# Optimization experiments

Measured on AMD Instinct MI355X. Metric: run time of the kernel, lower is better.

Reference implementation:

```python
import jax, jax.numpy as jnp
import numpy as np
from jax import lax

# program token ids
PAD, START, END, SCENE, INTERSECT, FILT, RELATE, QUERY = range(8)
SKIP = (PAD, START, END)


def conv2d(x, w, b, dil=1):
    # 'same' padding for odd kernels (3x3 pad=dil, 1x1 pad=0), NCHW/OIHW
    pad = dil * (w.shape[2] // 2)
    y = lax.conv_general_dilated(x, w, (1, 1), [(pad, pad), (pad, pad)],
                                 rhs_dilation=(dil, dil),
                                 dimension_numbers=('NCHW', 'OIHW', 'NCHW'))
    return y + b[None, :, None, None]


def maxpool2(x):
    return lax.reduce_window(x, -jnp.inf, lax.max, (1, 1, 2, 2), (1, 1, 2, 2), 'VALID')


def exec_program(prog, feat_input, p):
    """Run one (concrete) program over a batch of stem features. prog: tuple of ints,
    executed in reversed order exactly like TbDNet.forward."""
    B, _, H, W = feat_input.shape
    output = feat_input
    saved = None
    for t in reversed(prog):
        if t in SKIP:
            continue
        if t == SCENE:
            saved = output
            output = jnp.ones((B, 1, H, W), feat_input.dtype)
        elif t == INTERSECT:  # AndModule: elementwise min of attentions
            output = jnp.minimum(output, saved)
        elif t == FILT:
            a = feat_input * output  # [B,D,H,W] * [B,1,H,W]
            a = jax.nn.relu(conv2d(a, p['att_w1'], p['att_b1']))
            a = jax.nn.relu(conv2d(a, p['att_w2'], p['att_b2']))
            output = jax.nn.sigmoid(conv2d(a, p['att_w3'], p['att_b3']))
        elif t == RELATE:  # RelateModule: dilated conv stack (1,2,4,8,1) -> conv1x1 sigmoid
            a = feat_input * output
            for w, b, d in ((p['rel_w1'], p['rel_b1'], 1), (p['rel_w2'], p['rel_b2'], 2),
                            (p['rel_w3'], p['rel_b3'], 4), (p['rel_w4'], p['rel_b4'], 8),
                            (p['rel_w5'], p['rel_b5'], 1)):
                a = jax.nn.relu(conv2d(a, w, b, d))
            output = jax.nn.sigmoid(conv2d(a, p['rel_w6'], p['rel_b6']))
        elif t == QUERY:
            a = feat_input * output
            a = jax.nn.relu(conv2d(a, p['qry_w1'], p['qry_b1']))
            output = jax.nn.relu(conv2d(a, p['qry_w2'], p['qry_b2']))
    return output


def tbd_forward(feats, programs_np, p):
    B = feats.shape[0]
    stem = jax.nn.relu(conv2d(feats, p['stem_w1'], p['stem_b1']))
    stem = jax.nn.relu(conv2d(stem, p['stem_w2'], p['stem_b2']))  # [B,D,H,W]
    D, H, W = stem.shape[1], stem.shape[2], stem.shape[3]
    # group samples by identical program so dispatch runs batched, not per-sample
    groups = {}
    for n in range(B):
        groups.setdefault(tuple(int(v) for v in programs_np[n]), []).append(n)
    mod_out = jnp.zeros((B, D, H, W), feats.dtype)
    for prog, idxs in groups.items():
        idx = jnp.array(idxs)
        mod_out = mod_out.at[idx].set(exec_program(prog, stem[idx], p))
    # classifier: conv1x1 -> relu -> maxpool2 -> flatten -> fc -> relu -> fc
    x = jax.nn.relu(conv2d(mod_out, p['cls_w'], p['cls_b']))
    x = maxpool2(x)                        # [B,1024,7,7]
    x = x.reshape(B, -1)                   # [B,50176]
    x = jax.nn.relu(x @ p['fc1_w'].T + p['fc1_b'])
    return x @ p['fc2_w'].T + p['fc2_b']   # [B,28]


def setup_inputs() -> dict:
    key = jax.random.key(0)
    ks = iter(jax.random.split(key, 64))
    def rn(shape, s=0.05):
        return jax.random.normal(next(ks), shape, dtype=jnp.float32) * s
    B, Cin, H, W, D, P, L, A = 64, 1024, 14, 14, 128, 1024, 1024, 28
    feats = jax.random.normal(next(ks), (B, Cin, H, W), dtype=jnp.float32)
    # stored programs; execution order is reversed(stored)
    progA = [START, QUERY, FILT, RELATE, FILT, SCENE, END, PAD]            # scene->filter->relate->filter->query
    progB = [START, QUERY, INTERSECT, FILT, SCENE, FILT, SCENE, END]       # two filter branches -> intersect -> query
    programs = jnp.array([progA] * (B // 2) + [progB] * (B // 2), dtype=jnp.int32)
    inp = {'feats': feats, 'programs': programs,
           'stem_w1': rn((D, Cin, 3, 3), 0.02), 'stem_b1': rn((D,)),
           'stem_w2': rn((D, D, 3, 3)), 'stem_b2': rn((D,)),
           'att_w1': rn((D, D, 3, 3)), 'att_b1': rn((D,)),
           'att_w2': rn((D, D, 3, 3)), 'att_b2': rn((D,)),
           'att_w3': rn((1, D, 1, 1)), 'att_b3': rn((1,)),
           'rel_w1': rn((D, D, 3, 3)), 'rel_b1': rn((D,)),
           'rel_w2': rn((D, D, 3, 3)), 'rel_b2': rn((D,)),
           'rel_w3': rn((D, D, 3, 3)), 'rel_b3': rn((D,)),
           'rel_w4': rn((D, D, 3, 3)), 'rel_b4': rn((D,)),
           'rel_w5': rn((D, D, 3, 3)), 'rel_b5': rn((D,)),
           'rel_w6': rn((1, D, 1, 1)), 'rel_b6': rn((1,)),
           'qry_w1': rn((D, D, 3, 3)), 'qry_b1': rn((D,)),
           'qry_w2': rn((D, D, 3, 3)), 'qry_b2': rn((D,)),
           'cls_w': rn((P, D, 1, 1)), 'cls_b': rn((P,)),
           'fc1_w': rn((L, P * (H // 2) * (W // 2)), 0.01), 'fc1_b': rn((L,)),
           'fc2_w': rn((A, L)), 'fc2_b': rn((A,))}
    return inp


PARAM_NAMES = ['stem_w1', 'stem_b1', 'stem_w2', 'stem_b2',
               'att_w1', 'att_b1', 'att_w2', 'att_b2', 'att_w3', 'att_b3',
               'rel_w1', 'rel_b1', 'rel_w2', 'rel_b2', 'rel_w3', 'rel_b3',
               'rel_w4', 'rel_b4', 'rel_w5', 'rel_b5', 'rel_w6', 'rel_b6',
               'qry_w1', 'qry_b1', 'qry_w2', 'qry_b2',
               'cls_w', 'cls_b', 'fc1_w', 'fc1_b', 'fc2_w', 'fc2_b']


def reference(feats, programs, stem_w1, stem_b1, stem_w2, stem_b2,
              att_w1, att_b1, att_w2, att_b2, att_w3, att_b3,
              rel_w1, rel_b1, rel_w2, rel_b2, rel_w3, rel_b3,
              rel_w4, rel_b4, rel_w5, rel_b5, rel_w6, rel_b6,
              qry_w1, qry_b1, qry_w2, qry_b2,
              cls_w, cls_b, fc1_w, fc1_b, fc2_w, fc2_b):
    vals = [stem_w1, stem_b1, stem_w2, stem_b2,
            att_w1, att_b1, att_w2, att_b2, att_w3, att_b3,
            rel_w1, rel_b1, rel_w2, rel_b2, rel_w3, rel_b3,
            rel_w4, rel_b4, rel_w5, rel_b5, rel_w6, rel_b6,
            qry_w1, qry_b1, qry_w2, qry_b2,
            cls_w, cls_b, fc1_w, fc1_b, fc2_w, fc2_b]
    p = dict(zip(PARAM_NAMES, vals))
    return tbd_forward(feats, np.asarray(programs), p)
```

## Files before the change

kernel.cpp:

```cpp
#include <hip/hip_runtime.h>
#include <math.h>


typedef __attribute__((ext_vector_type(8)))  short   short8;
typedef __attribute__((ext_vector_type(8)))  __bf16  bf16x8;
typedef __attribute__((ext_vector_type(4)))  float   f32x4;

#define NROUNDS 11
#define NKS 98

#define B_WSTEM1 0UL
#define B_WSTEM2 2359296UL
#define B_WMOD   2654208UL
#define B_WCLS   5308416UL
#define B_STEM   5570560UL
#define B_XA     8781824UL
#define B_XB     11993088UL
#define B_FEAT   15204352UL
#define B_ATTN   18415616UL
#define B_SAVED  18465792UL
#define B_SCHED  18515968UL
#define B_ACTB   18520064UL
#define B_FC1T   24942592UL
#define B_P1X1   25204736UL
#define B_S1P    67108864UL
#define B_FC1P   100663296UL

__device__ __forceinline__ unsigned short f2bf(float f) {
    unsigned int b = __float_as_uint(f);
    b += 0x7fffu + ((b >> 16) & 1u);
    return (unsigned short)(b >> 16);
}
__device__ __forceinline__ float bf2f(unsigned short u) {
    return __uint_as_float(((unsigned int)u) << 16);
}
__device__ __forceinline__ f32x4 mfma16(bf16x8 a, bf16x8 b, f32x4 c) {
    return __builtin_amdgcn_mfma_f32_16x16x32_bf16(a, b, c, 0, 0, 0);
}

struct RepackArgs { const float* src[12]; };

__global__ __launch_bounds__(256) void k_repack(RepackArgs a, char* ws)
{
    const int y = blockIdx.y;
    const float* __restrict__ src = a.src[y];
    int gid = blockIdx.x * 256 + threadIdx.x;
    int gsz = gridDim.x * 256;
    if (y == 11) {
        unsigned short* dst = (unsigned short*)(ws + B_WCLS);
        for (int i = gid; i < 131072; i += gsz) dst[i] = f2bf(src[i]);
    } else {
        const int IC = (y == 0) ? 1024 : 128;
        const int lg = (y == 0) ? 10 : 7;
        unsigned short* dst = (unsigned short*)(ws + ((y == 0) ? B_WSTEM1
                                    : (y == 1) ? B_WSTEM2
                                    : B_WMOD + (size_t)(y - 2) * 294912));
        const int total = 9 << (lg + 7);
        for (int i = gid; i < total; i += gsz) {
            int ic = i & (IC - 1);
            int oc = (i >> lg) & 127;
            int t  = i >> (lg + 7);
            dst[i] = f2bf(src[((size_t)oc * IC + ic) * 9 + t]);
        }
    }
}

__global__ __launch_bounds__(256) void k_decode_init(const int* __restrict__ prog, char* ws)
{
    int gid = blockIdx.x * 256 + threadIdx.x;
    int gsz = gridDim.x * 256;
    float* attn  = (float*)(ws + B_ATTN);
    float* saved = (float*)(ws + B_SAVED);
    float* p1    = (float*)(ws + B_P1X1);
    for (int i = gid; i < 64 * 196; i += gsz) { attn[i] = 1.0f; saved[i] = 1.0f; }
    for (int i = gid; i < 8 * 64 * 196; i += gsz) p1[i] = 0.0f;
    unsigned int* fz = (unsigned int*)(ws + B_FEAT);
    for (int i = gid; i < 64 * 25088 / 2; i += gsz) fz[i] = 0u;
    if (gid < 64) {
        int n = gid;
        int ent[NROUNDS];
        for (int r = 0; r < NROUNDS; ++r) ent[r] = 0;
        int rc = 0, nslot = 0;
        int pscene = 0, pinter = 0, pmat = 0, pmw = 0;
#define PREBITS ((pscene<<17)|(pinter<<18)|(pmat<<19)|(pmw<<22))
#define CLRPRE  (pscene = pinter = pmat = pmw = 0)
#define EMIT(v) do { if (rc < NROUNDS) ent[rc++] = (v); } while (0)
        for (int j = 7; j >= 0; --j) {
            int t = prog[n * 8 + j];
            switch (t) {
                case 3: pscene = 1; break;
                case 4: pinter = 1; break;
                case 5: {
                    int e1 = 3 | (0<<4) | (1<<8) | (1<<12) | (2<<13) | (0<<15) | PREBITS;
                    CLRPRE; EMIT(e1);
                    EMIT(3 | (1<<4) | (1<<8) | (0<<12) | (0<<13) | (1<<15)
                           | (1<<23) | (0<<24) | (nslot<<25));
                    pmat = nslot + 1; pmw = 0; nslot++;
                    break;
                }
                case 6: {
                    int e1 = 3 | (2<<4) | (1<<8) | (1<<12) | (2<<13) | (0<<15) | PREBITS;
                    CLRPRE; EMIT(e1);
                    EMIT(3 | (3<<4) | (2<<8) | (0<<12) | (0<<13) | (1<<15));
                    EMIT(3 | (4<<4) | (4<<8) | (0<<12) | (1<<13) | (0<<15));
                    EMIT(3 | (5<<4) | (8<<8) | (0<<12) | (0<<13) | (1<<15));
                    EMIT(3 | (6<<4) | (1<<8) | (0<<12) | (1<<13) | (0<<15)
                           | (1<<23) | (1<<24) | (nslot<<25));
                    pmat = nslot + 1; pmw = 1; nslot++;
                    break;
                }
                case 7: {
                    int e1 = 3 | (7<<4) | (1<<8) | (1<<12) | (2<<13) | (0<<15) | PREBITS;
                    CLRPRE; EMIT(e1);
                    EMIT(3 | (8<<4) | (1<<8) | (0<<12) | (0<<13) | (2<<15));
                    break;
                }
                default: break;
            }
        }
#undef EMIT
#undef PREBITS
#undef CLRPRE
        int* sched = (int*)(ws + B_SCHED);
        for (int r = 0; r < NROUNDS; ++r) sched[n * NROUNDS + r] = ent[r];
    }
}

__global__ __launch_bounds__(512) void k_stem1p(const float* __restrict__ feats,
                                                const unsigned short* __restrict__ wrep,
                                                char* ws)
{
    __shared__ unsigned short s_img[197 * 136];
    const int bx = blockIdx.x;
    const int n = bx >> 3, ks = bx & 7;
    const int tid = threadIdx.x, lane = tid & 63;
    const int w = tid >> 6, wm = w & 1, wn = w >> 1;
    const int l15 = lane & 15, lq = lane >> 4;

    if (tid < 68) ((unsigned int*)s_img)[196 * 68 + tid] = 0u;

    int pglob[4], pbyt[4], pyv[4], pxv[4];
#pragma unroll
    for (int j = 0; j < 4; ++j) {
        int p  = (wn + 4 * j) * 16 + l15;
        pglob[j] = p;
        int py = p / 14;
        pyv[j] = (p < 196) ? py : 10000;
        pxv[j] = p - py * 14;
        pbyt[j] = p * 272 + lq * 16;
    }
    const int zaddr = 196 * 272 + lq * 16;
    const int nJ = (wn == 0) ? 4 : 3;

    f32x4 acc[4][4];
#pragma unroll
    for (int m = 0; m < 4; ++m)
#pragma unroll
        for (int j = 0; j < 4; ++j) acc[m][j] = (f32x4){0.f, 0.f, 0.f, 0.f};

    const int icg = tid & 31;
    const int qq0 = tid >> 5;
    const int icb = ks * 128;

    const float* sf = feats + ((size_t)n * 1024 + icb) * 196;
    for (int qq = qq0; qq < 49; qq += 16) {
        const float* p0 = sf + icg * 4 * 196 + qq * 4;
        float4 r0 = *(const float4*)(p0);
        float4 r1 = *(const float4*)(p0 + 196);
        float4 r2 = *(const float4*)(p0 + 392);
        float4 r3 = *(const float4*)(p0 + 588);
#pragma unroll
        for (int e = 0; e < 4; ++e) {
            uint2 v;
            v.x = (unsigned int)f2bf(((const float*)&r0)[e]) |
                  ((unsigned int)f2bf(((const float*)&r1)[e]) << 16);
            v.y = (unsigned int)f2bf(((const float*)&r2)[e]) |
                  ((unsigned int)f2bf(((const float*)&r3)[e]) << 16);
            *(uint2*)(s_img + (qq * 4 + e) * 136 + icg * 4) = v;
        }
    }
    __syncthreads();

#pragma unroll
    for (int t = 0; t < 9; ++t) {
        const int dy = t / 3 - 1, dx = t % 3 - 1;
        int baddr[4];
#pragma unroll
        for (int j = 0; j < 4; ++j) {
            int yy = pyv[j] + dy, xx = pxv[j] + dx;
            bool ok = ((unsigned)yy < 14u) && ((unsigned)xx < 14u);
            baddr[j] = ok ? (pbyt[j] + (dy * 14 + dx) * 272) : zaddr;
        }
#pragma unroll
        for (int kc = 0; kc < 4; ++kc) {
            const unsigned short* wt = wrep +
                ((size_t)(t * 128 + wm * 64 + l15) * 1024 + icb + kc * 32 + lq * 8);
            bf16x8 am[4];
#pragma unroll
            for (int m = 0; m < 4; ++m)
                am[m] = *(const bf16x8*)(wt + (size_t)m * 16 * 1024);
#pragma unroll
            for (int j = 0; j < 4; ++j) {
                if (j < nJ) {
                    bf16x8 b = *(const bf16x8*)((const char*)s_img + baddr[j] + kc * 64);
#pragma unroll
                    for (int m = 0; m < 4; ++m)
                        acc[m][j] = mfma16(am[m], b, acc[m][j]);
                }
            }
        }
    }

    unsigned short* part = (unsigned short*)(ws + B_S1P);
#pragma unroll
    for (int m = 0; m < 4; ++m) {
        const int oc = wm * 64 + m * 16 + lq * 4;
#pragma unroll
        for (int j = 0; j < 4; ++j) {
            if (j < nJ) {
                int p = pglob[j];
                if (p < 196) {
                    unsigned int lo = (unsigned int)f2bf(acc[m][j][0]) |
                                      ((unsigned int)f2bf(acc[m][j][1]) << 16);
                    unsigned int hi = (unsigned int)f2bf(acc[m][j][2]) |
                                      ((unsigned int)f2bf(acc[m][j][3]) << 16);
                    uint2 pk; pk.x = lo; pk.y = hi;
                    *(uint2*)(part + (((size_t)ks * 64 + n) * 196 + p) * 128 + oc) = pk;
                }
            }
        }
    }
}

__global__ __launch_bounds__(256) void k_stem1r(const char* __restrict__ ws_c,
                                                const float* __restrict__ bias,
                                                unsigned short* __restrict__ xa)
{
    int i = blockIdx.x * 256 + threadIdx.x;
    const unsigned short* part = (const unsigned short*)(ws_c + B_S1P);
    int oc8 = (i & 15) * 8;
    int np  = i >> 4;
    float s[8] = {};
#pragma unroll
    for (int ks = 0; ks < 8; ++ks) {
        short8 v = *(const short8*)(part + (((size_t)ks * 64) * 196 + np) * 128 + oc8);
#pragma unroll
        for (int e = 0; e < 8; ++e) s[e] += bf2f((unsigned short)v[e]);
    }
    short8 o;
#pragma unroll
    for (int e = 0; e < 8; ++e)
        o[e] = (short)f2bf(fmaxf(s[e] + bias[oc8 + e], 0.f));
    *(short8*)(xa + (size_t)np * 128 + oc8) = o;
}

__device__ void conv_core32(const unsigned short* __restrict__ srcB,
                            const float* __restrict__ s_gate,
                            const unsigned short* __restrict__ wrep,
                            const float* __restrict__ bias,
                            unsigned short* __restrict__ dst,
                            int dil, int oct, int pxh,
                            unsigned short* s_img,
                            int post, const float* __restrict__ pwv,
                            float* __restrict__ pdst)
{
    const int tid  = threadIdx.x, lane = tid & 63;
    const int w    = tid >> 6, wm = w & 1, wn = w >> 1;
    const int l15  = lane & 15, lq = lane >> 4;

    if (tid < 68) ((unsigned int*)s_img)[196 * 68 + tid] = 0u;

    int pglob[4], pbyt[4], pyv[4], pxv[4];
#pragma unroll
    for (int j = 0; j < 4; ++j) {
        int nt = wn + 2 * j;
        int p  = (pxh * 7 + nt) * 16 + l15;
        pglob[j] = p;
        int py = p / 14;
        pyv[j] = (p < 196) ? py : 10000;
        pxv[j] = p - py * 14;
        pbyt[j] = p * 272 + lq * 16;
    }
    const int zaddr = 196 * 272 + lq * 16;
    const int nNT = (wn == 0) ? 4 : 3;

    f32x4 acc[4];
#pragma unroll
    for (int j = 0; j < 4; ++j) acc[j] = (f32x4){0.f, 0.f, 0.f, 0.f};

    if (s_gate) {
        for (int i = tid; i < 196 * 16; i += 256) {
            int p = i >> 4, c8 = (i & 15) * 8;
            short8 v = *(const short8*)(srcB + p * 128 + c8);
            float g = s_gate[p];
            short8 ov;
#pragma unroll
            for (int e = 0; e < 8; ++e)
                ov[e] = (short)f2bf(bf2f((unsigned short)v[e]) * g);
            *(short8*)(s_img + p * 136 + c8) = ov;
        }
    } else {
        for (int i = tid; i < 196 * 16; i += 256) {
            int p = i >> 4, c8 = (i & 15) * 8;
            *(short8*)(s_img + p * 136 + c8) = *(const short8*)(srcB + p * 128 + c8);
        }
    }
    __syncthreads();

    const unsigned short* wlane = wrep + (size_t)(oct * 32 + wm * 16 + l15) * 128 + lq * 8;
#pragma unroll
    for (int t = 0; t < 9; ++t) {
        const int dy = (t / 3 - 1) * dil, dx = (t % 3 - 1) * dil;
        int baddr[4];
#pragma unroll
        for (int j = 0; j < 4; ++j) {
            int yy = pyv[j] + dy, xx = pxv[j] + dx;
            bool ok = ((unsigned)yy < 14u) && ((unsigned)xx < 14u);
            baddr[j] = ok ? (pbyt[j] + (dy * 14 + dx) * 272) : zaddr;
        }
        const unsigned short* wt = wlane + (size_t)(t * 128) * 128;
#pragma unroll
        for (int kc = 0; kc < 4; ++kc) {
            bf16x8 a0 = *(const bf16x8*)(wt + kc * 32);
#pragma unroll
            for (int j = 0; j < 4; ++j) {
                if (j < nNT) {
                    bf16x8 b = *(const bf16x8*)((const char*)s_img + baddr[j] + kc * 64);
                    acc[j] = mfma16(a0, b, acc[j]);
                }
            }
        }
    }

    const int oc = oct * 32 + wm * 16 + lq * 4;
    const float4 b4 = *(const float4*)(bias + oc);
    float4 wv4;
    if (post) wv4 = *(const float4*)(pwv + oc);
#pragma unroll
    for (int j = 0; j < 4; ++j) {
        if (j < nNT) {
            int p = pglob[j];
            if (p < 196) {
                float v0 = fmaxf(acc[j][0] + b4.x, 0.f);
                float v1 = fmaxf(acc[j][1] + b4.y, 0.f);
                float v2 = fmaxf(acc[j][2] + b4.z, 0.f);
                float v3 = fmaxf(acc[j][3] + b4.w, 0.f);
                uint2 pk;
                pk.x = (unsigned int)f2bf(v0) | ((unsigned int)f2bf(v1) << 16);
                pk.y = (unsigned int)f2bf(v2) | ((unsigned int)f2bf(v3) << 16);
                *(uint2*)(dst + p * 128 + oc) = pk;
                if (post) {
                    float s = v0 * wv4.x + v1 * wv4.y + v2 * wv4.z + v3 * wv4.w;
                    atomicAdd(pdst + p, s);
                }
            }
        }
    }
}

__global__ __launch_bounds__(256) void k_conv_stem2(const unsigned short* __restrict__ srcBall,
                                                    const unsigned short* __restrict__ wrep,
                                                    const float* __restrict__ bias,
                                                    unsigned short* __restrict__ dstall)
{
    __shared__ unsigned short s_img[197 * 136];
    const int n = blockIdx.x >> 3, oct = (blockIdx.x >> 1) & 3, pxh = blockIdx.x & 1;
    conv_core32(srcBall + (size_t)n * 25088, nullptr, wrep, bias,
                dstall + (size_t)n * 25088, 1, oct, pxh, s_img, 0, nullptr, nullptr);
}

struct RArgs {
    char* ws;
    const float* mbias[9];
    const float* w1x1[2];
    const float* b1x1[2];
};

__global__ __launch_bounds__(256) void k_round(RArgs a, int r)
{
    __shared__ unsigned short s_img[197 * 136];
    __shared__ float s_gate[196];
    const int bx = blockIdx.x;
    const int n = bx >> 3, oct = (bx >> 1) & 3, pxh = bx & 1;
    char* ws = a.ws;
    const int* sched = (const int*)(ws + B_SCHED);
    const int e = sched[n * NROUNDS + r];
    if ((e & 15) == 0) return;
    const int tid = threadIdx.x;
    const int wset = (e >> 4) & 15, dil = (e >> 8) & 15, gatef = (e >> 12) & 1;
    const int srcid = (e >> 13) & 3, dstid = (e >> 15) & 3;
    const int fscene = (e >> 17) & 1, finter = (e >> 18) & 1;
    const int mslot = (e >> 19) & 7, mw = (e >> 22) & 1;
    const int post = (e >> 23) & 1, pw = (e >> 24) & 1, pslot = (e >> 25) & 7;

    float* attn  = (float*)(ws + B_ATTN)  + n * 196;
    float* saved = (float*)(ws + B_SAVED) + n * 196;
    float* p1    = (float*)(ws + B_P1X1);

    if (gatef) {
        if (tid < 196) {
            float cur = attn[tid];
            if (mslot) {
                float pv = p1[(size_t)(mslot - 1) * 12544 + n * 196 + tid];
                cur = 1.0f / (1.0f + __expf(-(pv + a.b1x1[mw][0])));
            }
            if (fscene) { saved[tid] = cur; cur = 1.0f; }
            if (finter) { cur = fminf(cur, saved[tid]); }
            if (mslot | fscene | finter) attn[tid] = cur;
            s_gate[tid] = cur;
        }
        __syncthreads();
    }

    const unsigned short* src = (const unsigned short*)(ws +
            (srcid == 2 ? B_STEM : srcid == 1 ? B_XB : B_XA)) + (size_t)n * 25088;
    unsigned short* dst = (unsigned short*)(ws +
            (dstid == 2 ? B_FEAT : dstid == 1 ? B_XB : B_XA)) + (size_t)n * 25088;
    const unsigned short* wrep = (const unsigned short*)(ws + B_WMOD) + (size_t)wset * 9 * 128 * 128;

    conv_core32(src, gatef ? s_gate : nullptr, wrep, a.mbias[wset], dst,
                dil, oct, pxh, s_img,
                post, post ? a.w1x1[pw] : nullptr,
                post ? (p1 + (size_t)pslot * 12544 + n * 196) : nullptr);
}

__global__ __launch_bounds__(256) void k_cls_pool(const unsigned short* __restrict__ featall,
                                                  const unsigned short* __restrict__ clsw,
                                                  const float* __restrict__ clsb,
                                                  unsigned short* __restrict__ actB)
{
    __shared__ char smem[197 * 272 + 64 * 200 * 4];
    unsigned short* s_img = (unsigned short*)smem;
    float* s_pool = (float*)(smem + 197 * 272);
    const int n = blockIdx.x >> 4, pt = blockIdx.x & 15;
    const int tid = threadIdx.x, lane = tid & 63, w = tid >> 6;
    const int l15 = lane & 15, lq = lane >> 4;
    const unsigned short* feat = featall + (size_t)n * 25088;

    if (tid < 68) ((unsigned int*)s_img)[196 * 68 + tid] = 0u;
    for (int i = tid; i < 196 * 16; i += 256) {
        int p = i >> 4, c8 = (i & 15) * 8;
        *(short8*)(s_img + p * 136 + c8) = *(const short8*)(feat + p * 128 + c8);
    }
    f32x4 acc[14];
#pragma unroll
    for (int j = 0; j < 14; ++j) acc[j] = (f32x4){0.f, 0.f, 0.f, 0.f};
    __syncthreads();

    const unsigned short* wl = clsw + (size_t)(pt * 64 + w * 16 + l15) * 128 + lq * 8;
#pragma unroll
    for (int kc = 0; kc < 4; ++kc) {
        bf16x8 a0 = *(const bf16x8*)(wl + kc * 32);
#pragma unroll
        for (int j = 0; j < 14; ++j) {
            int p = j * 16 + l15;
            int ba = (p < 196) ? (p * 272 + lq * 16 + kc * 64) : (196 * 272 + lq * 16);
            bf16x8 b = *(const bf16x8*)((const char*)s_img + ba);
            acc[j] = mfma16(a0, b, acc[j]);
        }
    }
    const int oc = pt * 64 + w * 16 + lq * 4;
    const float4 b4 = *(const float4*)(clsb + oc);
    const int pl = w * 16 + lq * 4;
#pragma unroll
    for (int j = 0; j < 14; ++j) {
        int p = j * 16 + l15;
        if (p < 196) {
            s_pool[(pl + 0) * 200 + p] = fmaxf(acc[j][0] + b4.x, 0.f);
            s_pool[(pl + 1) * 200 + p] = fmaxf(acc[j][1] + b4.y, 0.f);
            s_pool[(pl + 2) * 200 + p] = fmaxf(acc[j][2] + b4.z, 0.f);
            s_pool[(pl + 3) * 200 + p] = fmaxf(acc[j][3] + b4.w, 0.f);
        }
    }
    __syncthreads();
    for (int i = tid; i < 64 * 49; i += 256) {
        int plx = i / 49, q = i - plx * 49;
        int py = q / 7, qx = q - py * 7;
        const float* rp = s_pool + plx * 200 + py * 28 + qx * 2;
        float m = fmaxf(fmaxf(rp[0], rp[1]), fmaxf(rp[14], rp[15]));
        int k = (pt * 64 + plx) * 49 + q;
        int kb = k >> 6, lq2 = (k >> 4) & 3, hi = (k >> 3) & 1, e = k & 7;
        actB[((((size_t)kb * 4 + lq2) * 2 + hi) * 64 + n) * 8 + e] = f2bf(m);
    }
}

__global__ __launch_bounds__(256) void k_fc1p(const unsigned short* __restrict__ actB,
                                              const float* __restrict__ w,
                                              float* __restrict__ part)
{
    __shared__ unsigned short s_w[64 * 264];
    const int jt = blockIdx.x & 15, ks = blockIdx.x >> 4;
    const int tid = threadIdx.x, lane = tid & 63, wv = tid >> 6;
    const int l15 = lane & 15, lq = lane >> 4;
    const int k0 = ks * 512;

    f32x4 acc[4];
#pragma unroll
    for (int t = 0; t < 4; ++t) acc[t] = (f32x4){0.f, 0.f, 0.f, 0.f};

    float4 pf[16];

#define FC1_LOAD(ss_) do {                                                        \
    _Pragma("unroll")                                                             \
    for (int pass = 0; pass < 16; ++pass) {                                       \
        const int row_ = pass * 4 + wv;                                           \
        pf[pass] = *(const float4*)(w + (size_t)(jt * 64 + row_) * 50176 + k0     \
                                      + (ss_) * 256 + lane * 4);                  \
    } } while (0)

    FC1_LOAD(0);

    for (int ss = 0; ss < 2; ++ss) {
        __syncthreads();
#pragma unroll
        for (int pass = 0; pass < 16; ++pass) {
            const int row = pass * 4 + wv;
            uint2 v;
            v.x = (unsigned int)f2bf(pf[pass].x) | ((unsigned int)f2bf(pf[pass].y) << 16);
            v.y = (unsigned int)f2bf(pf[pass].z) | ((unsigned int)f2bf(pf[pass].w) << 16);
            *(uint2*)(s_w + row * 264 + lane * 4) = v;
        }
        __syncthreads();
        if (ss < 1) FC1_LOAD(1);

        const unsigned short* arow = s_w + (wv * 16 + l15) * 264;
#pragma unroll
        for (int kk = 0; kk < 8; ++kk) {
            bf16x8 a = *(const bf16x8*)(arow + kk * 32 + lq * 8);
            const int kglob = k0 + ss * 256 + kk * 32 + lq * 8;
            const int kb = kglob >> 6, lq2 = (kglob >> 4) & 3, hi = (kglob >> 3) & 1;
            const unsigned short* bp = actB +
                ((((size_t)kb * 4 + lq2) * 2 + hi) * 64 + l15) * 8;
#pragma unroll
            for (int t = 0; t < 4; ++t) {
                bf16x8 b = *(const bf16x8*)(bp + t * 128);
                acc[t] = mfma16(a, b, acc[t]);
            }
        }
    }
#undef FC1_LOAD

    float* pbase = part + ((size_t)ks * 1024 + jt * 64 + wv * 16 + lq * 4) * 64 + l15;
#pragma unroll
    for (int t = 0; t < 4; ++t)
#pragma unroll
        for (int r = 0; r < 4; ++r)
            pbase[(size_t)r * 64 + t * 16] = acc[t][r];
}

__global__ __launch_bounds__(256) void k_fc1r(const float* __restrict__ part,
                                              const float* __restrict__ b,
                                              float* __restrict__ fc1T)
{
    int i = blockIdx.x * 256 + threadIdx.x;
    if (i >= 65536) return;
    float s = 0.0f;
    for (int ks = 0; ks < NKS; ++ks) s += part[(size_t)ks * 65536 + i];
    int j = i >> 6;
    fc1T[i] = fmaxf(s + b[j], 0.0f);
}

__global__ __launch_bounds__(256) void k_fc2(const float* __restrict__ fc1T,
                                             const float* __restrict__ w,
                                             const float* __restrict__ b,
                                             float* __restrict__ out)
{
    __shared__ float red[256];
    const int a_ = blockIdx.x;
    const int tid = threadIdx.x, lane = tid & 63, q = tid >> 6;
    float acc = 0.0f;
    const float* wr = w + (size_t)a_ * 1024;
    for (int k = q * 256; k < q * 256 + 256; ++k)
        acc = fmaf(fc1T[k * 64 + lane], wr[k], acc);
    red[tid] = acc;
    __syncthreads();
    if (q == 0) {
        float s = red[tid] + red[tid + 64] + red[tid + 128] + red[tid + 192] + b[a_];
        out[lane * 28 + a_] = s;
    }
}

extern "C" void kernel_launch(void* const* d_in, const int* in_sizes, int n_in,
                              void* d_out, int out_size, void* d_ws, size_t ws_size,
                              hipStream_t stream)
{
    const float* feats = (const float*)d_in[0];
    const int*   prog  = (const int*)d_in[1];
    char* ws  = (char*)d_ws;
    float* out = (float*)d_out;

    RepackArgs ra;
    ra.src[0]  = (const float*)d_in[2];
    ra.src[1]  = (const float*)d_in[4];
    ra.src[2]  = (const float*)d_in[6];
    ra.src[3]  = (const float*)d_in[8];
    ra.src[4]  = (const float*)d_in[12];
    ra.src[5]  = (const float*)d_in[14];
    ra.src[6]  = (const float*)d_in[16];
    ra.src[7]  = (const float*)d_in[18];
    ra.src[8]  = (const float*)d_in[20];
    ra.src[9]  = (const float*)d_in[24];
    ra.src[10] = (const float*)d_in[26];
    ra.src[11] = (const float*)d_in[28];

    k_repack<<<dim3(64, 12), 256, 0, stream>>>(ra, ws);
    k_decode_init<<<256, 256, 0, stream>>>(prog, ws);

    k_stem1p<<<512, 512, 0, stream>>>(feats, (const unsigned short*)(ws + B_WSTEM1), ws);
    k_stem1r<<<784, 256, 0, stream>>>(ws, (const float*)d_in[3],
                                      (unsigned short*)(ws + B_XA));

    k_conv_stem2<<<512, 256, 0, stream>>>((const unsigned short*)(ws + B_XA),
                                          (const unsigned short*)(ws + B_WSTEM2),
                                          (const float*)d_in[5],
                                          (unsigned short*)(ws + B_STEM));

    RArgs ga;
    ga.ws = ws;
    ga.mbias[0] = (const float*)d_in[7];
    ga.mbias[1] = (const float*)d_in[9];
    ga.mbias[2] = (const float*)d_in[13];
    ga.mbias[3] = (const float*)d_in[15];
    ga.mbias[4] = (const float*)d_in[17];
    ga.mbias[5] = (const float*)d_in[19];
    ga.mbias[6] = (const float*)d_in[21];
    ga.mbias[7] = (const float*)d_in[25];
    ga.mbias[8] = (const float*)d_in[27];
    ga.w1x1[0]  = (const float*)d_in[10];
    ga.w1x1[1]  = (const float*)d_in[22];
    ga.b1x1[0]  = (const float*)d_in[11];
    ga.b1x1[1]  = (const float*)d_in[23];

    for (int r = 0; r < NROUNDS; ++r)
        k_round<<<512, 256, 0, stream>>>(ga, r);

    k_cls_pool<<<1024, 256, 0, stream>>>((const unsigned short*)(ws + B_FEAT),
                                         (const unsigned short*)(ws + B_WCLS),
                                         (const float*)d_in[29],
                                         (unsigned short*)(ws + B_ACTB));
    k_fc1p<<<1568, 256, 0, stream>>>((const unsigned short*)(ws + B_ACTB),
                                     (const float*)d_in[30], (float*)(ws + B_FC1P));
    k_fc1r<<<256, 256, 0, stream>>>((const float*)(ws + B_FC1P), (const float*)d_in[31],
                                    (float*)(ws + B_FC1T));
    k_fc2<<<28, 256, 0, stream>>>((const float*)(ws + B_FC1T), (const float*)d_in[32],
                                  (const float*)d_in[33], out);
}
```

Before: 511.4 us.

## Merge repack and decode kernels; stream fc1 weights directly into LDS

Combines the weight-repack and program-decode/init kernels into one launch, split by block index, which removes a kernel launch. In the fc1 partial GEMM, the register-staged fp32 weight loads with convert-then-store are replaced by global_load_lds direct-to-LDS transfers. These use an XOR-swizzled fp32 layout and four 128-wide k stages, and the bf16 conversion happens when the MFMA operands are read. This trades the register prefetch overlap for fewer VGPRs and direct async copies, but LDS traffic doubles because fp32 is kept there, and there is no double buffering.

```diff
diff --git a/kernel.cpp b/kernel.cpp
--- a/kernel.cpp
+++ b/kernel.cpp
@@ -38,37 +38,38 @@
     return __builtin_amdgcn_mfma_f32_16x16x32_bf16(a, b, c, 0, 0, 0);
 }
 
-struct RepackArgs { const float* src[12]; };
-
-__global__ __launch_bounds__(256) void k_repack(RepackArgs a, char* ws)
-{
-    const int y = blockIdx.y;
-    const float* __restrict__ src = a.src[y];
-    int gid = blockIdx.x * 256 + threadIdx.x;
-    int gsz = gridDim.x * 256;
-    if (y == 11) {
-        unsigned short* dst = (unsigned short*)(ws + B_WCLS);
-        for (int i = gid; i < 131072; i += gsz) dst[i] = f2bf(src[i]);
-    } else {
-        const int IC = (y == 0) ? 1024 : 128;
-        const int lg = (y == 0) ? 10 : 7;
-        unsigned short* dst = (unsigned short*)(ws + ((y == 0) ? B_WSTEM1
-                                    : (y == 1) ? B_WSTEM2
-                                    : B_WMOD + (size_t)(y - 2) * 294912));
-        const int total = 9 << (lg + 7);
-        for (int i = gid; i < total; i += gsz) {
-            int ic = i & (IC - 1);
-            int oc = (i >> lg) & 127;
-            int t  = i >> (lg + 7);
-            dst[i] = f2bf(src[((size_t)oc * IC + ic) * 9 + t]);
-        }
-    }
-}
-
-__global__ __launch_bounds__(256) void k_decode_init(const int* __restrict__ prog, char* ws)
-{
-    int gid = blockIdx.x * 256 + threadIdx.x;
-    int gsz = gridDim.x * 256;
+struct PrepArgs { const float* src[12]; const int* prog; char* ws; };
+
+__global__ __launch_bounds__(256) void k_prep(PrepArgs a)
+{
+    char* ws = a.ws;
+    const int bx = blockIdx.x;
+    if (bx < 768) {
+        const int y = bx >> 6;
+        const float* __restrict__ src = a.src[y];
+        int gid = (bx & 63) * 256 + threadIdx.x;
+        int gsz = 64 * 256;
+        if (y == 11) {
+            unsigned short* dst = (unsigned short*)(ws + B_WCLS);
+            for (int i = gid; i < 131072; i += gsz) dst[i] = f2bf(src[i]);
+        } else {
+            const int IC = (y == 0) ? 1024 : 128;
+            const int lg = (y == 0) ? 10 : 7;
+            unsigned short* dst = (unsigned short*)(ws + ((y == 0) ? B_WSTEM1
+                                        : (y == 1) ? B_WSTEM2
+                                        : B_WMOD + (size_t)(y - 2) * 294912));
+            const int total = 9 << (lg + 7);
+            for (int i = gid; i < total; i += gsz) {
+                int ic = i & (IC - 1);
+                int oc = (i >> lg) & 127;
+                int t  = i >> (lg + 7);
+                dst[i] = f2bf(src[((size_t)oc * IC + ic) * 9 + t]);
+            }
+        }
+        return;
+    }
+    int gid = (bx - 768) * 256 + threadIdx.x;
+    int gsz = 256 * 256;
     float* attn  = (float*)(ws + B_ATTN);
     float* saved = (float*)(ws + B_SAVED);
     float* p1    = (float*)(ws + B_P1X1);
@@ -78,6 +79,7 @@
     for (int i = gid; i < 64 * 25088 / 2; i += gsz) fz[i] = 0u;
     if (gid < 64) {
         int n = gid;
+        const int* prog = a.prog;
         int ent[NROUNDS];
         for (int r = 0; r < NROUNDS; ++r) ent[r] = 0;
         int rc = 0, nslot = 0;
@@ -488,7 +490,7 @@
                                               const float* __restrict__ w,
                                               float* __restrict__ part)
 {
-    __shared__ unsigned short s_w[64 * 264];
+    __shared__ float s_w[64 * 128];
     const int jt = blockIdx.x & 15, ks = blockIdx.x >> 4;
     const int tid = threadIdx.x, lane = tid & 63, wv = tid >> 6;
     const int l15 = lane & 15, lq = lane >> 4;
@@ -498,36 +500,38 @@
 #pragma unroll
     for (int t = 0; t < 4; ++t) acc[t] = (f32x4){0.f, 0.f, 0.f, 0.f};
 
-    float4 pf[16];
-
-#define FC1_LOAD(ss_) do {                                                        \
-    _Pragma("unroll")                                                             \
-    for (int pass = 0; pass < 16; ++pass) {                                       \
-        const int row_ = pass * 4 + wv;                                           \
-        pf[pass] = *(const float4*)(w + (size_t)(jt * 64 + row_) * 50176 + k0     \
-                                      + (ss_) * 256 + lane * 4);                  \
-    } } while (0)
-
-    FC1_LOAD(0);
-
-    for (int ss = 0; ss < 2; ++ss) {
+    const int half  = lane >> 5;
+    const int chunk = lane & 31;
+    const int srow  = wv * 16 + l15;
+    const int ssw   = srow & 7;
+    const float* arow = s_w + srow * 128;
+    const float* wbase = w + (size_t)(jt * 64) * 50176 + k0;
+
+    for (int st = 0; st < 4; ++st) {
         __syncthreads();
 #pragma unroll
-        for (int pass = 0; pass < 16; ++pass) {
-            const int row = pass * 4 + wv;
-            uint2 v;
-            v.x = (unsigned int)f2bf(pf[pass].x) | ((unsigned int)f2bf(pf[pass].y) << 16);
-            v.y = (unsigned int)f2bf(pf[pass].z) | ((unsigned int)f2bf(pf[pass].w) << 16);
-            *(uint2*)(s_w + row * 264 + lane * 4) = v;
+        for (int i = 0; i < 8; ++i) {
+            const int r0 = wv * 16 + i * 2;
+            const int rr = r0 + half;
+            const int g  = chunk ^ (rr & 7);
+            const float* src = wbase + (size_t)rr * 50176 + st * 128 + g * 4;
+            __builtin_amdgcn_global_load_lds(
+                (const __attribute__((address_space(1))) unsigned int*)src,
+                (__attribute__((address_space(3))) unsigned int*)(s_w + r0 * 128),
+                16, 0, 0);
         }
         __syncthreads();
-        if (ss < 1) FC1_LOAD(1);
-
-        const unsigned short* arow = s_w + (wv * 16 + l15) * 264;
-#pragma unroll
-        for (int kk = 0; kk < 8; ++kk) {
-            bf16x8 a = *(const bf16x8*)(arow + kk * 32 + lq * 8);
-            const int kglob = k0 + ss * 256 + kk * 32 + lq * 8;
+
+        const int kbase = k0 + st * 128;
+#pragma unroll
+        for (int kk = 0; kk < 4; ++kk) {
+            const int u0 = kk * 8 + lq * 2;
+            float4 f0 = *(const float4*)(arow + ((u0 ^ ssw) << 2));
+            float4 f1 = *(const float4*)(arow + (((u0 + 1) ^ ssw) << 2));
+            bf16x8 a;
+            a[0] = (__bf16)f0.x; a[1] = (__bf16)f0.y; a[2] = (__bf16)f0.z; a[3] = (__bf16)f0.w;
+            a[4] = (__bf16)f1.x; a[5] = (__bf16)f1.y; a[6] = (__bf16)f1.z; a[7] = (__bf16)f1.w;
+            const int kglob = kbase + kk * 32 + lq * 8;
             const int kb = kglob >> 6, lq2 = (kglob >> 4) & 3, hi = (kglob >> 3) & 1;
             const unsigned short* bp = actB +
                 ((((size_t)kb * 4 + lq2) * 2 + hi) * 64 + l15) * 8;
@@ -538,7 +542,6 @@
             }
         }
     }
-#undef FC1_LOAD
 
     float* pbase = part + ((size_t)ks * 1024 + jt * 64 + wv * 16 + lq * 4) * 64 + l15;
 #pragma unroll
@@ -589,22 +592,22 @@
     char* ws  = (char*)d_ws;
     float* out = (float*)d_out;
 
-    RepackArgs ra;
-    ra.src[0]  = (const float*)d_in[2];
-    ra.src[1]  = (const float*)d_in[4];
-    ra.src[2]  = (const float*)d_in[6];
-    ra.src[3]  = (const float*)d_in[8];
-    ra.src[4]  = (const float*)d_in[12];
-    ra.src[5]  = (const float*)d_in[14];
-    ra.src[6]  = (const float*)d_in[16];
-    ra.src[7]  = (const float*)d_in[18];
-    ra.src[8]  = (const float*)d_in[20];
-    ra.src[9]  = (const float*)d_in[24];
-    ra.src[10] = (const float*)d_in[26];
-    ra.src[11] = (const float*)d_in[28];
-
-    k_repack<<<dim3(64, 12), 256, 0, stream>>>(ra, ws);
-    k_decode_init<<<256, 256, 0, stream>>>(prog, ws);
+    PrepArgs pa;
+    pa.src[0]  = (const float*)d_in[2];
+    pa.src[1]  = (const float*)d_in[4];
+    pa.src[2]  = (const float*)d_in[6];
+    pa.src[3]  = (const float*)d_in[8];
+    pa.src[4]  = (const float*)d_in[12];
+    pa.src[5]  = (const float*)d_in[14];
+    pa.src[6]  = (const float*)d_in[16];
+    pa.src[7]  = (const float*)d_in[18];
+    pa.src[8]  = (const float*)d_in[20];
+    pa.src[9]  = (const float*)d_in[24];
+    pa.src[10] = (const float*)d_in[26];
+    pa.src[11] = (const float*)d_in[28];
+    pa.prog = prog;
+    pa.ws = ws;
+    k_prep<<<1024, 256, 0, stream>>>(pa);
 
     k_stem1p<<<512, 512, 0, stream>>>(feats, (const unsigned short*)(ws + B_WSTEM1), ws);
     k_stem1r<<<784, 256, 0, stream>>>(ws, (const float*)d_in[3],
```

Measured after the change: 527.7 us. 3.2% more time.
